# Kernel tuning notes

Measured on AMD Instinct MI355X. Metric: run time of the kernel, lower is better.

## Reference

```python
import jax, jax.numpy as jnp
import numpy as np

NUM_HEADS = 8
AGENT_NUM = 16
POOL = 4  # sqrt(agent_num)


def _block_pool(t, b, H, W, c):
    # AdaptiveAvgPool2d to (POOL, POOL); H, W divisible by POOL -> exact block mean.
    # t: (b, n, c) with n = H*W, spatial layout reshape(b, H, W, c)
    hb, wb = H // POOL, W // POOL
    t = t.reshape(b, POOL, hb, POOL, wb, c)
    return t.mean(axis=(2, 4)).reshape(b, AGENT_NUM, c)  # (b, agent_num, c)


def setup_inputs() -> dict:
    key = jax.random.key(0)
    ks = jax.random.split(key, 6)
    b, H, W, c = 32, 56, 56, 384
    n = H * W
    return {
        "x": jax.random.normal(ks[0], (b, n, c), dtype=jnp.float32),
        "H": H,
        "W": W,
        "Wq": jax.random.normal(ks[1], (c, c), dtype=jnp.float32) * 0.02,
        "Wkv": jax.random.normal(ks[2], (c, c), dtype=jnp.float32) * 0.02,
        "w_g": jax.random.normal(ks[3], (c, 1), dtype=jnp.float32) * 0.02,
        "Wp": jax.random.normal(ks[4], (c, c), dtype=jnp.float32) * 0.02,
        "bp": jax.random.normal(ks[5], (c,), dtype=jnp.float32) * 0.02,
    }


def reference(x, H, W, Wq, Wkv, w_g, Wp, bp):
    b, n, c = x.shape
    h, d = NUM_HEADS, c // NUM_HEADS
    scale = d ** -0.5

    q = x @ Wq.T            # (b, n, c)  q = Linear(x), no bias
    k = x @ Wkv.T           # (b, n, c)  kv = Linear(x), sr_ratio == 1

    agent_q = _block_pool(q, b, H, W, c)   # (b, agent_num, c)
    agent_k = _block_pool(k, b, H, W, c)   # (b, agent_num, c)

    # gating: A = (agent_q @ w_g) * scale; G = sum(A * agent_q, dim=1)
    A = (agent_q @ w_g) * scale                    # (b, agent_num, 1)
    G = jnp.sum(A * agent_q, axis=1)               # (b, c)
    agent_new = (G[:, None, :] * agent_k) @ Wp.T + bp + agent_q  # (b, agent_num, c)

    # split heads
    qh = q.reshape(b, n, h, d).transpose(0, 2, 1, 3)               # (b, h, n, d)
    an = agent_new.reshape(b, AGENT_NUM, h, d).transpose(0, 2, 1, 3)  # (b, h, a, d)
    ak = agent_k.reshape(b, AGENT_NUM, h, d).transpose(0, 2, 1, 3)    # (b, h, a, d)

    q_attn = jax.nn.softmax(jnp.einsum('bhnd,bhad->bhna', qh * scale, an), axis=-1)
    out = jnp.einsum('bhna,bhad->bhnd', q_attn, ak)                # (b, h, n, d)
    out = out.transpose(0, 2, 1, 3).reshape(b, n, c)
    return out @ Wp.T + bp  # Proj reused for output projection
```

## Files before the change

### kernel.cpp

```cpp
#include <hip/hip_runtime.h>
#include <hip/hip_bf16.h>
#include <cstdint>
#include <cstddef>

#define NB   32
#define NPOS 3136
#define NC   384
#define NHD  8
#define DH   48
#define NAG  16
#define MROWS (NB*NPOS)
#define CQK  768

static constexpr float kScale = 0.14433756729740643f;
static constexpr float kInv196 = 1.0f / 196.0f;

typedef __bf16 bf16x8 __attribute__((ext_vector_type(8)));
typedef float  f32x4  __attribute__((ext_vector_type(4)));

__device__ static inline void async_copy16(void* lds, const void* g) {
    __builtin_amdgcn_global_load_lds(
        (const __attribute__((address_space(1))) unsigned int*)g,
        (__attribute__((address_space(3))) unsigned int*)lds, 16, 0, 0);
}

__global__ __launch_bounds__(256) void cvt4_kernel(const float* __restrict__ src,
                                                   __hip_bfloat16* __restrict__ dst,
                                                   int n4) {
    int i = blockIdx.x * 256 + threadIdx.x;
    if (i >= n4) return;
    float4 v = ((const float4*)src)[i];
    union { ushort4 u; __hip_bfloat16 h[4]; } p;
    p.h[0] = __float2bfloat16(v.x);
    p.h[1] = __float2bfloat16(v.y);
    p.h[2] = __float2bfloat16(v.z);
    p.h[3] = __float2bfloat16(v.w);
    ((ushort4*)dst)[i] = p.u;
}

template<bool HAS_BIAS, bool OUT_BF16, bool RESID>
__global__ __launch_bounds__(256) void gemm_kernel(
    const __hip_bfloat16* __restrict__ A,
    const __hip_bfloat16* __restrict__ Bw,
    const float* __restrict__ bias,
    const float* __restrict__ resid,
    void* __restrict__ Cout,
    int nBlkN, int Nn, int K)
{
    __shared__ unsigned char smem[32768];
    unsigned char* smA = smem;
    unsigned char* smB = smem + 16384;

    const int t    = threadIdx.x;
    const int m0   = (blockIdx.x / nBlkN) * 128;
    const int n0   = (blockIdx.x % nBlkN) * 128;
    const int lane = t & 63;
    const int w    = t >> 6;
    const int wm   = (w >> 1) * 64;
    const int wn   = (w & 1) * 64;
    const int lr   = lane & 15;
    const int lg   = lane >> 4;

    const int Kb    = K << 1;
    const int lrow  = lane >> 3;
    const int lslot = ((lane & 7) ^ lrow) << 4;
    const char* Ag = (const char*)A  + (size_t)(m0 + 32 * w + lrow) * Kb + lslot;
    const char* Bg = (const char*)Bw + (size_t)(n0 + 32 * w + lrow) * Kb + lslot;
    unsigned char* ldsA = smA + w * 4096;
    unsigned char* ldsB = smB + w * 4096;

    f32x4 acc[4][4] = {};

    const int nk = K >> 6;
    for (int kt = 0; kt < nk; ++kt) {
        __syncthreads();
        #pragma unroll
        for (int j = 0; j < 4; ++j) {
            async_copy16(ldsA + j * 1024, Ag + (size_t)(8 * j) * Kb);
            async_copy16(ldsB + j * 1024, Bg + (size_t)(8 * j) * Kb);
        }
        Ag += 128; Bg += 128;
        __syncthreads();

        #pragma unroll
        for (int kk = 0; kk < 2; ++kk) {
            bf16x8 av[4], bv[4];
            #pragma unroll
            for (int mf = 0; mf < 4; ++mf) {
                const int row = wm + mf * 16 + lr;
                av[mf] = *(const bf16x8*)(smA + row * 128 + ((((kk << 2) | lg) ^ (row & 7)) << 4));
            }
            #pragma unroll
            for (int nf = 0; nf < 4; ++nf) {
                const int row = wn + nf * 16 + lr;
                bv[nf] = *(const bf16x8*)(smB + row * 128 + ((((kk << 2) | lg) ^ (row & 7)) << 4));
            }
            #pragma unroll
            for (int mf = 0; mf < 4; ++mf)
                #pragma unroll
                for (int nf = 0; nf < 4; ++nf)
                    acc[mf][nf] = __builtin_amdgcn_mfma_f32_16x16x32_bf16(av[mf], bv[nf], acc[mf][nf], 0, 0, 0);
        }
    }

    #pragma unroll
    for (int mf = 0; mf < 4; ++mf) {
        #pragma unroll
        for (int nf = 0; nf < 4; ++nf) {
            #pragma unroll
            for (int j = 0; j < 4; ++j) {
                int row = m0 + wm + mf * 16 + (lg << 2) + j;
                int col = n0 + wn + nf * 16 + lr;
                float v = acc[mf][nf][j];
                if (HAS_BIAS) v += bias[col];
                if (RESID)    v += resid[(size_t)row * Nn + col];
                if (OUT_BF16)
                    ((__hip_bfloat16*)Cout)[(size_t)row * Nn + col] = __float2bfloat16(v);
                else
                    ((float*)Cout)[(size_t)row * Nn + col] = v;
            }
        }
    }
}

__global__ __launch_bounds__(256) void pool_kernel(const __hip_bfloat16* __restrict__ qk,
                                                   float* __restrict__ agent_qk) {
    int idx = blockIdx.x * 256 + threadIdx.x;
    int ch4 = (idx % 192) * 4;
    int a   = (idx / 192) & 15;
    int b   = idx / 3072;
    int py = a >> 2, px = a & 3;
    const __hip_bfloat16* base = qk + (size_t)b * NPOS * CQK + ch4;
    float s0 = 0.f, s1 = 0.f, s2 = 0.f, s3 = 0.f;
    for (int dy = 0; dy < 14; ++dy) {
        int rowbase = (py * 14 + dy) * 56 + px * 14;
        #pragma unroll
        for (int dx = 0; dx < 14; ++dx) {
            union { uint2 u; __hip_bfloat16 h[4]; } v;
            v.u = *(const uint2*)(base + (size_t)(rowbase + dx) * CQK);
            s0 += (float)v.h[0];
            s1 += (float)v.h[1];
            s2 += (float)v.h[2];
            s3 += (float)v.h[3];
        }
    }
    float4 o;
    o.x = s0 * kInv196; o.y = s1 * kInv196; o.z = s2 * kInv196; o.w = s3 * kInv196;
    ((float4*)agent_qk)[idx] = o;
}

__global__ __launch_bounds__(256) void agent_prep_kernel(
    const float* __restrict__ agqk,
    const float* __restrict__ w_g,
    __hip_bfloat16* __restrict__ gkb,
    __hip_bfloat16* __restrict__ akb,
    float* __restrict__ aqf)
{
    __shared__ float aq[NAG][NC];
    __shared__ float Av[NAG];
    __shared__ float G[NC];
    const int b = blockIdx.x, t = threadIdx.x;
    const float* base = agqk + (size_t)b * NAG * CQK;

    for (int i = t; i < NAG * NC; i += 256) {
        int a = i / NC, cc = i - a * NC;
        aq[a][cc] = base[a * CQK + cc];
    }
    __syncthreads();

    {
        int a = t >> 4, l = t & 15;
        float s = 0.f;
        for (int cc = l; cc < NC; cc += 16) s += aq[a][cc] * w_g[cc];
        s += __shfl_down(s, 8, 16);
        s += __shfl_down(s, 4, 16);
        s += __shfl_down(s, 2, 16);
        s += __shfl_down(s, 1, 16);
        if (l == 0) Av[a] = s * kScale;
    }
    __syncthreads();

    for (int cc = t; cc < NC; cc += 256) {
        float s = 0.f;
        #pragma unroll
        for (int a = 0; a < NAG; ++a) s += Av[a] * aq[a][cc];
        G[cc] = s;
    }
    __syncthreads();

    for (int i = t; i < NAG * NC; i += 256) {
        int a = i / NC, cc = i - a * NC;
        float kv = base[a * CQK + NC + cc];
        size_t o = (size_t)b * NAG * NC + i;
        akb[o] = __float2bfloat16(kv);
        gkb[o] = __float2bfloat16(G[cc] * kv);
        aqf[o] = aq[a][cc];
    }
}

__global__ __launch_bounds__(256) void attn_kernel(
    const __hip_bfloat16* __restrict__ qk,
    const __hip_bfloat16* __restrict__ anb,
    const __hip_bfloat16* __restrict__ akb,
    __hip_bfloat16* __restrict__ outb)
{
    const int bh = blockIdx.x;
    const int b = bh >> 3, hd = bh & 7;
    __shared__ float an_s[NAG][DH];
    __shared__ float ak_s[NAG][DH];
    const int t = threadIdx.x;
    for (int i = t; i < NAG * DH; i += 256) {
        int a = i / DH, dd = i - a * DH;
        an_s[a][dd] = (float)anb[((size_t)b * NAG + a) * NC + hd * DH + dd];
        ak_s[a][dd] = (float)akb[((size_t)b * NAG + a) * NC + hd * DH + dd];
    }
    __syncthreads();
    const int row = blockIdx.y * 256 + t;
    if (row >= NPOS) return;

    union { uint4 u[6]; __hip_bfloat16 h[48]; } qv;
    const uint4* qp = (const uint4*)(qk + ((size_t)b * NPOS + row) * CQK + hd * DH);
    #pragma unroll
    for (int i = 0; i < 6; ++i) qv.u[i] = qp[i];
    float qf[DH];
    #pragma unroll
    for (int dd = 0; dd < DH; ++dd) qf[dd] = (float)qv.h[dd];

    float sv[NAG];
    float mx = -1e30f;
    #pragma unroll
    for (int a = 0; a < NAG; ++a) {
        float s = 0.f;
        #pragma unroll
        for (int dd = 0; dd < DH; ++dd) s += qf[dd] * an_s[a][dd];
        s *= kScale;
        sv[a] = s;
        mx = fmaxf(mx, s);
    }
    float den = 0.f;
    #pragma unroll
    for (int a = 0; a < NAG; ++a) { sv[a] = __expf(sv[a] - mx); den += sv[a]; }
    const float inv = 1.f / den;

    float o[DH];
    #pragma unroll
    for (int dd = 0; dd < DH; ++dd) o[dd] = 0.f;
    #pragma unroll
    for (int a = 0; a < NAG; ++a) {
        float p = sv[a] * inv;
        #pragma unroll
        for (int dd = 0; dd < DH; ++dd) o[dd] += p * ak_s[a][dd];
    }

    union { uint4 u[6]; __hip_bfloat16 h[48]; } ov;
    #pragma unroll
    for (int dd = 0; dd < DH; ++dd) ov.h[dd] = __float2bfloat16(o[dd]);
    uint4* op = (uint4*)(outb + ((size_t)b * NPOS + row) * NC + hd * DH);
    #pragma unroll
    for (int i = 0; i < 6; ++i) op[i] = ov.u[i];
}

extern "C" void kernel_launch(void* const* d_in, const int* in_sizes, int n_in,
                              void* d_out, int out_size, void* d_ws, size_t ws_size,
                              hipStream_t stream) {
    (void)in_sizes; (void)n_in; (void)out_size; (void)ws_size;
    const float* x   = (const float*)d_in[0];
    const float* Wq  = (const float*)d_in[3];
    const float* Wkv = (const float*)d_in[4];
    const float* wg  = (const float*)d_in[5];
    const float* Wp  = (const float*)d_in[6];
    const float* bp  = (const float*)d_in[7];
    float* out = (float*)d_out;

    char* w = (char*)d_ws;
    __hip_bfloat16* xb   = (__hip_bfloat16*)(w);
    __hip_bfloat16* qkb  = (__hip_bfloat16*)(w + 77070336);
    __hip_bfloat16* wqkb = (__hip_bfloat16*)(w + 231211008);
    __hip_bfloat16* wpb  = (__hip_bfloat16*)(w + 231800832);
    float*          agqk = (float*)(w + 232095744);
    __hip_bfloat16* anb  = (__hip_bfloat16*)(w + 233668608);
    __hip_bfloat16* akb  = (__hip_bfloat16*)(w + 234061824);

    __hip_bfloat16* gkb = (__hip_bfloat16*)(w);
    float*          aqf = (float*)(w + 393216);

    cvt4_kernel<<<37632, 256, 0, stream>>>(x, xb, 9633792);
    cvt4_kernel<<<144, 256, 0, stream>>>(Wq,  wqkb,          36864);
    cvt4_kernel<<<144, 256, 0, stream>>>(Wkv, wqkb + 147456, 36864);
    cvt4_kernel<<<144, 256, 0, stream>>>(Wp,  wpb,           36864);

    gemm_kernel<false, true, false><<<(MROWS / 128) * (CQK / 128), 256, 0, stream>>>(
        xb, wqkb, nullptr, nullptr, qkb, CQK / 128, CQK, NC);

    pool_kernel<<<384, 256, 0, stream>>>(qkb, agqk);

    agent_prep_kernel<<<NB, 256, 0, stream>>>(agqk, wg, gkb, akb, aqf);

    gemm_kernel<true, true, true><<<4 * 3, 256, 0, stream>>>(
        gkb, wpb, bp, aqf, anb, NC / 128, NC, NC);

    attn_kernel<<<dim3(NB * NHD, (NPOS + 255) / 256), 256, 0, stream>>>(qkb, anb, akb, xb);

    gemm_kernel<true, false, false><<<(MROWS / 128) * (NC / 128), 256, 0, stream>>>(
        xb, wpb, bp, nullptr, out, NC / 128, NC, NC);
}
```

Baseline: 533.0 us.

## Fuse x conversion and pooling into QK GEMM, fold agent projection into prep kernel

The QK projection GEMM now reads fp32 x directly and converts it to bf16 in registers, which removes the separate 154MB x conversion pass. Its epilogue block-pools the accumulators into agent sums through LDS and global atomics, replacing the separate pool kernel that reread qk. The three weight conversions and the zeroing of the pool buffer are merged into one setup kernel. The small agent projection GEMM is folded into the agent prep kernel using MFMA, and the GEMMs use an XCD-aware block remap. The costs are fp32 A loads that are no longer asynchronous, atomic contention in the epilogue, and a float summation order that is no longer deterministic.

```diff
diff --git a/kernel.cpp b/kernel.cpp
--- a/kernel.cpp
+++ b/kernel.cpp
@@ -24,36 +24,54 @@
         (__attribute__((address_space(3))) unsigned int*)lds, 16, 0, 0);
 }
 
-__global__ __launch_bounds__(256) void cvt4_kernel(const float* __restrict__ src,
-                                                   __hip_bfloat16* __restrict__ dst,
-                                                   int n4) {
-    int i = blockIdx.x * 256 + threadIdx.x;
-    if (i >= n4) return;
-    float4 v = ((const float4*)src)[i];
-    union { ushort4 u; __hip_bfloat16 h[4]; } p;
-    p.h[0] = __float2bfloat16(v.x);
-    p.h[1] = __float2bfloat16(v.y);
-    p.h[2] = __float2bfloat16(v.z);
-    p.h[3] = __float2bfloat16(v.w);
-    ((ushort4*)dst)[i] = p.u;
-}
-
-template<bool HAS_BIAS, bool OUT_BF16, bool RESID>
+__global__ __launch_bounds__(256) void setup_kernel(
+    const float* __restrict__ Wq, const float* __restrict__ Wkv,
+    const float* __restrict__ Wp,
+    __hip_bfloat16* __restrict__ wqkb, __hip_bfloat16* __restrict__ wpb,
+    float* __restrict__ agqk)
+{
+    const int bid = blockIdx.x, t = threadIdx.x;
+    if (bid < 432) {
+        const float* src; __hip_bfloat16* dst; int lb = bid;
+        if (lb < 144)      { src = Wq;  dst = wqkb; }
+        else if (lb < 288) { src = Wkv; dst = wqkb + 147456; lb -= 144; }
+        else               { src = Wp;  dst = wpb;           lb -= 288; }
+        int i = lb * 256 + t;
+        float4 v = ((const float4*)src)[i];
+        union { ushort4 u; __hip_bfloat16 h[4]; } p;
+        p.h[0] = __float2bfloat16(v.x);
+        p.h[1] = __float2bfloat16(v.y);
+        p.h[2] = __float2bfloat16(v.z);
+        p.h[3] = __float2bfloat16(v.w);
+        ((ushort4*)dst)[i] = p.u;
+    } else {
+        int i = (bid - 432) * 256 + t;
+        float4 z; z.x = z.y = z.z = z.w = 0.f;
+        ((float4*)agqk)[i] = z;
+    }
+}
+
+template<bool HAS_BIAS, bool OUT_BF16, bool A_F32, bool POOL>
 __global__ __launch_bounds__(256) void gemm_kernel(
-    const __hip_bfloat16* __restrict__ A,
+    const void* __restrict__ Ap,
     const __hip_bfloat16* __restrict__ Bw,
     const float* __restrict__ bias,
-    const float* __restrict__ resid,
     void* __restrict__ Cout,
+    float* __restrict__ poolbuf,
     int nBlkN, int Nn, int K)
 {
     __shared__ unsigned char smem[32768];
     unsigned char* smA = smem;
     unsigned char* smB = smem + 16384;
 
-    const int t    = threadIdx.x;
-    const int m0   = (blockIdx.x / nBlkN) * 128;
-    const int n0   = (blockIdx.x % nBlkN) * 128;
+    const int t = threadIdx.x;
+    const int nwg = gridDim.x;
+    const int qq = nwg >> 3, rr = nwg & 7;
+    const int xcd = blockIdx.x & 7, sidx0 = blockIdx.x >> 3;
+    const int wgid = (xcd < rr ? xcd * (qq + 1) : rr * (qq + 1) + (xcd - rr) * qq) + sidx0;
+    const int m0 = (wgid / nBlkN) * 128;
+    const int n0 = (wgid % nBlkN) * 128;
+
     const int lane = t & 63;
     const int w    = t >> 6;
     const int wm   = (w >> 1) * 64;
@@ -64,22 +82,52 @@
     const int Kb    = K << 1;
     const int lrow  = lane >> 3;
     const int lslot = ((lane & 7) ^ lrow) << 4;
-    const char* Ag = (const char*)A  + (size_t)(m0 + 32 * w + lrow) * Kb + lslot;
+    const char* Ag = A_F32 ? nullptr
+                   : (const char*)Ap + (size_t)(m0 + 32 * w + lrow) * Kb + lslot;
     const char* Bg = (const char*)Bw + (size_t)(n0 + 32 * w + lrow) * Kb + lslot;
     unsigned char* ldsA = smA + w * 4096;
     unsigned char* ldsB = smB + w * 4096;
 
+    const int ar = t >> 1, ah = t & 1;
+    const float* Af = A_F32 ? (const float*)Ap + (size_t)(m0 + ar) * K + ah * 32 : nullptr;
+
     f32x4 acc[4][4] = {};
 
     const int nk = K >> 6;
     for (int kt = 0; kt < nk; ++kt) {
-        __syncthreads();
-        #pragma unroll
-        for (int j = 0; j < 4; ++j) {
-            async_copy16(ldsA + j * 1024, Ag + (size_t)(8 * j) * Kb);
-            async_copy16(ldsB + j * 1024, Bg + (size_t)(8 * j) * Kb);
-        }
-        Ag += 128; Bg += 128;
+        float4 af[8];
+        if (A_F32) {
+            const float4* s4 = (const float4*)(Af + kt * 64);
+            #pragma unroll
+            for (int j = 0; j < 8; ++j) af[j] = s4[j];
+        }
+        __syncthreads();
+        if (A_F32) {
+            union { bf16x8 v[4]; __hip_bfloat16 h[32]; } cv;
+            #pragma unroll
+            for (int j = 0; j < 8; ++j) {
+                cv.h[4 * j + 0] = __float2bfloat16(af[j].x);
+                cv.h[4 * j + 1] = __float2bfloat16(af[j].y);
+                cv.h[4 * j + 2] = __float2bfloat16(af[j].z);
+                cv.h[4 * j + 3] = __float2bfloat16(af[j].w);
+            }
+            #pragma unroll
+            for (int qc = 0; qc < 4; ++qc) {
+                int sl = (((ah << 2) | qc) ^ (ar & 7)) << 4;
+                *(bf16x8*)(smA + ar * 128 + sl) = cv.v[qc];
+            }
+            #pragma unroll
+            for (int j = 0; j < 4; ++j)
+                async_copy16(ldsB + j * 1024, Bg + (size_t)(8 * j) * Kb);
+            Bg += 128;
+        } else {
+            #pragma unroll
+            for (int j = 0; j < 4; ++j) {
+                async_copy16(ldsA + j * 1024, Ag + (size_t)(8 * j) * Kb);
+                async_copy16(ldsB + j * 1024, Bg + (size_t)(8 * j) * Kb);
+            }
+            Ag += 128; Bg += 128;
+        }
         __syncthreads();
 
         #pragma unroll
@@ -113,7 +161,6 @@
                 int col = n0 + wn + nf * 16 + lr;
                 float v = acc[mf][nf][j];
                 if (HAS_BIAS) v += bias[col];
-                if (RESID)    v += resid[(size_t)row * Nn + col];
                 if (OUT_BF16)
                     ((__hip_bfloat16*)Cout)[(size_t)row * Nn + col] = __float2bfloat16(v);
                 else
@@ -121,42 +168,50 @@
             }
         }
     }
-}
-
-__global__ __launch_bounds__(256) void pool_kernel(const __hip_bfloat16* __restrict__ qk,
-                                                   float* __restrict__ agent_qk) {
-    int idx = blockIdx.x * 256 + threadIdx.x;
-    int ch4 = (idx % 192) * 4;
-    int a   = (idx / 192) & 15;
-    int b   = idx / 3072;
-    int py = a >> 2, px = a & 3;
-    const __hip_bfloat16* base = qk + (size_t)b * NPOS * CQK + ch4;
-    float s0 = 0.f, s1 = 0.f, s2 = 0.f, s3 = 0.f;
-    for (int dy = 0; dy < 14; ++dy) {
-        int rowbase = (py * 14 + dy) * 56 + px * 14;
-        #pragma unroll
-        for (int dx = 0; dx < 14; ++dx) {
-            union { uint2 u; __hip_bfloat16 h[4]; } v;
-            v.u = *(const uint2*)(base + (size_t)(rowbase + dx) * CQK);
-            s0 += (float)v.h[0];
-            s1 += (float)v.h[1];
-            s2 += (float)v.h[2];
-            s3 += (float)v.h[3];
-        }
-    }
-    float4 o;
-    o.x = s0 * kInv196; o.y = s1 * kInv196; o.z = s2 * kInv196; o.w = s3 * kInv196;
-    ((float4*)agent_qk)[idx] = o;
-}
-
-__global__ __launch_bounds__(256) void agent_prep_kernel(
+
+    if (POOL) {
+        __syncthreads();
+        float (*ps)[4][128] = (float (*)[4][128])smem;
+        for (int i = t; i < 1024; i += 256) ((float*)ps)[i] = 0.f;
+        __syncthreads();
+        const int base784 = m0 / 784;
+        #pragma unroll
+        for (int mf = 0; mf < 4; ++mf) {
+            #pragma unroll
+            for (int nf = 0; nf < 4; ++nf) {
+                #pragma unroll
+                for (int j = 0; j < 4; ++j) {
+                    int r  = m0 + wm + mf * 16 + (lg << 2) + j;
+                    int s  = (r / 784) - base784;
+                    int px = (r % 56) / 14;
+                    int cl = wn + nf * 16 + lr;
+                    atomicAdd(&ps[s][px][cl], acc[mf][nf][j]);
+                }
+            }
+        }
+        __syncthreads();
+        for (int i = t; i < 1024; i += 256) {
+            int s = i >> 9, px = (i >> 7) & 3, cl = i & 127;
+            int r784 = base784 + s;
+            if (r784 < 128) {
+                int b = r784 >> 2, py = r784 & 3;
+                atomicAdd(&poolbuf[(size_t)(b * NAG + py * 4 + px) * CQK + n0 + cl],
+                          ps[s][px][cl]);
+            }
+        }
+    }
+}
+
+__global__ __launch_bounds__(256) void agent_fused_kernel(
     const float* __restrict__ agqk,
     const float* __restrict__ w_g,
-    __hip_bfloat16* __restrict__ gkb,
-    __hip_bfloat16* __restrict__ akb,
-    float* __restrict__ aqf)
+    const __hip_bfloat16* __restrict__ wpb,
+    const float* __restrict__ bp,
+    __hip_bfloat16* __restrict__ anb,
+    __hip_bfloat16* __restrict__ akb)
 {
     __shared__ float aq[NAG][NC];
+    __shared__ __hip_bfloat16 gks[NAG][NC + 8];
     __shared__ float Av[NAG];
     __shared__ float G[NC];
     const int b = blockIdx.x, t = threadIdx.x;
@@ -164,7 +219,7 @@
 
     for (int i = t; i < NAG * NC; i += 256) {
         int a = i / NC, cc = i - a * NC;
-        aq[a][cc] = base[a * CQK + cc];
+        aq[a][cc] = base[a * CQK + cc] * kInv196;
     }
     __syncthreads();
 
@@ -190,11 +245,32 @@
 
     for (int i = t; i < NAG * NC; i += 256) {
         int a = i / NC, cc = i - a * NC;
-        float kv = base[a * CQK + NC + cc];
-        size_t o = (size_t)b * NAG * NC + i;
-        akb[o] = __float2bfloat16(kv);
-        gkb[o] = __float2bfloat16(G[cc] * kv);
-        aqf[o] = aq[a][cc];
+        float kv = base[a * CQK + NC + cc] * kInv196;
+        akb[(size_t)b * NAG * NC + i] = __float2bfloat16(kv);
+        gks[a][cc] = __float2bfloat16(G[cc] * kv);
+    }
+    __syncthreads();
+
+    const int lane = t & 63, wv = t >> 6, lr = lane & 15, lg = lane >> 4;
+    f32x4 acc[6] = {};
+    for (int ks = 0; ks < 12; ++ks) {
+        bf16x8 av = *(const bf16x8*)&gks[lr][ks * 32 + lg * 8];
+        #pragma unroll
+        for (int nf = 0; nf < 6; ++nf) {
+            int ncol = wv * 96 + nf * 16 + lr;
+            bf16x8 bv = *(const bf16x8*)(wpb + (size_t)ncol * NC + ks * 32 + lg * 8);
+            acc[nf] = __builtin_amdgcn_mfma_f32_16x16x32_bf16(av, bv, acc[nf], 0, 0, 0);
+        }
+    }
+    #pragma unroll
+    for (int nf = 0; nf < 6; ++nf) {
+        #pragma unroll
+        for (int j = 0; j < 4; ++j) {
+            int agent = (lg << 2) + j;
+            int ncol  = wv * 96 + nf * 16 + lr;
+            float v = acc[nf][j] + bp[ncol] + aq[agent][ncol];
+            anb[((size_t)b * NAG + agent) * NC + ncol] = __float2bfloat16(v);
+        }
     }
 }
 
@@ -273,7 +349,7 @@
     float* out = (float*)d_out;
 
     char* w = (char*)d_ws;
-    __hip_bfloat16* xb   = (__hip_bfloat16*)(w);
+    __hip_bfloat16* aout = (__hip_bfloat16*)(w);
     __hip_bfloat16* qkb  = (__hip_bfloat16*)(w + 77070336);
     __hip_bfloat16* wqkb = (__hip_bfloat16*)(w + 231211008);
     __hip_bfloat16* wpb  = (__hip_bfloat16*)(w + 231800832);
@@ -281,26 +357,15 @@
     __hip_bfloat16* anb  = (__hip_bfloat16*)(w + 233668608);
     __hip_bfloat16* akb  = (__hip_bfloat16*)(w + 234061824);
 
-    __hip_bfloat16* gkb = (__hip_bfloat16*)(w);
-    float*          aqf = (float*)(w + 393216);
-
-    cvt4_kernel<<<37632, 256, 0, stream>>>(x, xb, 9633792);
-    cvt4_kernel<<<144, 256, 0, stream>>>(Wq,  wqkb,          36864);
-    cvt4_kernel<<<144, 256, 0, stream>>>(Wkv, wqkb + 147456, 36864);
-    cvt4_kernel<<<144, 256, 0, stream>>>(Wp,  wpb,           36864);
-
-    gemm_kernel<false, true, false><<<(MROWS / 128) * (CQK / 128), 256, 0, stream>>>(
-        xb, wqkb, nullptr, nullptr, qkb, CQK / 128, CQK, NC);
-
-    pool_kernel<<<384, 256, 0, stream>>>(qkb, agqk);
-
-    agent_prep_kernel<<<NB, 256, 0, stream>>>(agqk, wg, gkb, akb, aqf);
-
-    gemm_kernel<true, true, true><<<4 * 3, 256, 0, stream>>>(
-        gkb, wpb, bp, aqf, anb, NC / 128, NC, NC);
-
-    attn_kernel<<<dim3(NB * NHD, (NPOS + 255) / 256), 256, 0, stream>>>(qkb, anb, akb, xb);
-
-    gemm_kernel<true, false, false><<<(MROWS / 128) * (NC / 128), 256, 0, stream>>>(
-        xb, wpb, bp, nullptr, out, NC / 128, NC, NC);
-}
+    setup_kernel<<<816, 256, 0, stream>>>(Wq, Wkv, Wp, wqkb, wpb, agqk);
+
+    gemm_kernel<false, true, true, true><<<(MROWS / 128) * (CQK / 128), 256, 0, stream>>>(
+        x, wqkb, nullptr, qkb, agqk, CQK / 128, CQK, NC);
+
+    agent_fused_kernel<<<NB, 256, 0, stream>>>(agqk, wg, wpb, bp, anb, akb);
+
+    attn_kernel<<<dim3(NB * NHD, (NPOS + 255) / 256), 256, 0, stream>>>(qkb, anb, akb, aout);
+
+    gemm_kernel<true, false, false, false><<<(MROWS / 128) * (NC / 128), 256, 0, stream>>>(
+        aout, wpb, bp, out, nullptr, NC / 128, NC, NC);
+}
```

Result: slower. 948.2 us (+77.9%).
